# Kernel optimization log

Measured on AMD Instinct MI355X. Metric: run time of the kernel, lower is better.

## Reference

```python
import jax, jax.numpy as jnp
import numpy as np

SEQ_LEN, BATCH = 512, 64
VOCAB, EMB, HID = 10000, 512, 512


def _lstm_layer(x, Wih, Whh, bih, bhh):
    # x: [T, B, in_dim]; PyTorch gate order: i, f, g, o
    T, B, _ = x.shape
    H = Whh.shape[1]
    b = bih + bhh
    # precompute input projections for all timesteps: [T, B, 4H]
    xW = jnp.einsum('tbe,ge->tbg', x, Wih) + b

    def step(carry, xt):
        h, c = carry
        gates = xt + h @ Whh.T  # [B, 4H]
        i, f, g, o = jnp.split(gates, 4, axis=-1)
        i = jax.nn.sigmoid(i)
        f = jax.nn.sigmoid(f)
        g = jnp.tanh(g)
        o = jax.nn.sigmoid(o)
        c = f * c + i * g
        h = o * jnp.tanh(c)
        return (h, c), h

    init = (jnp.zeros((B, H), x.dtype), jnp.zeros((B, H), x.dtype))
    _, ys = jax.lax.scan(step, init, xW)
    return ys  # [T, B, H]


def setup_inputs() -> dict:
    key = jax.random.key(0)
    ks = jax.random.split(key, 12)
    src = jax.random.randint(ks[0], (SEQ_LEN, BATCH), 0, VOCAB)
    sen_len = jax.random.randint(ks[1], (BATCH,), 1, SEQ_LEN + 1)
    s_e = 1.0 / np.sqrt(EMB)
    s_h = 1.0 / np.sqrt(HID)
    emb_table = jax.random.normal(ks[2], (VOCAB, EMB), jnp.float32) * s_e
    Wih0 = jax.random.uniform(ks[3], (4 * HID, EMB), jnp.float32, -s_h, s_h)
    Whh0 = jax.random.uniform(ks[4], (4 * HID, HID), jnp.float32, -s_h, s_h)
    bih0 = jax.random.uniform(ks[5], (4 * HID,), jnp.float32, -s_h, s_h)
    bhh0 = jax.random.uniform(ks[6], (4 * HID,), jnp.float32, -s_h, s_h)
    Wih1 = jax.random.uniform(ks[7], (4 * HID, HID), jnp.float32, -s_h, s_h)
    Whh1 = jax.random.uniform(ks[8], (4 * HID, HID), jnp.float32, -s_h, s_h)
    bih1 = jax.random.uniform(ks[9], (4 * HID,), jnp.float32, -s_h, s_h)
    bhh1 = jax.random.uniform(ks[10], (4 * HID,), jnp.float32, -s_h, s_h)
    return {"src": src, "sen_len": sen_len, "emb_table": emb_table,
            "Wih0": Wih0, "Whh0": Whh0, "bih0": bih0, "bhh0": bhh0,
            "Wih1": Wih1, "Whh1": Whh1, "bih1": bih1, "bhh1": bhh1}


def reference(src, sen_len, emb_table, Wih0, Whh0, bih0, bhh0, Wih1, Whh1, bih1, bhh1):
    # Vectorized embedding gather: [T, B, EMB]
    embedded = emb_table[src]
    # Two-layer LSTM (eval mode; inter-layer dropout inactive)
    h1 = _lstm_layer(embedded, Wih0, Whh0, bih0, bhh0)
    outputs = _lstm_layer(h1, Wih1, Whh1, bih1, bhh1)  # [T, B, HID]
    # Per-sequence last valid hidden state, concatenated into flat vector [B*HID]
    B = src.shape[1]
    ot = outputs[sen_len - 1, jnp.arange(B), :]  # [B, HID]
    return ot.reshape(-1)
```

## Files before the change

### kernel.cpp

```cpp
#include <hip/hip_runtime.h>

#define T_LEN 512
#define BATCH 64
#define HID   512
#define EMB   512
#define NWG   256
#define TPB   512
#define RING_SLOT (HID * BATCH)

struct GBar {
  int leaf[16 * 32];
  int root; int pad1[31];
  int epoch; int pad2[31];
  int gep[16 * 32];
};

__global__ void init_ws_kernel(int* ws, int n) {
  int stride = gridDim.x * blockDim.x;
  for (int i = blockIdx.x * blockDim.x + threadIdx.x; i < n; i += stride) ws[i] = 0;
}

__device__ __forceinline__ float sigm(float x)      { return 1.f / (1.f + __expf(-x)); }
__device__ __forceinline__ float tanh_fast(float x) { return 1.f - 2.f / (__expf(2.f * x) + 1.f); }

__device__ __forceinline__ void cstore(float* p, float v) {
  __hip_atomic_store(p, v, __ATOMIC_RELAXED, __HIP_MEMORY_SCOPE_AGENT);
}

template <int I, int N>
struct Issue16 {
  static __device__ __forceinline__ void go(float4* dst, const float* p) {
    asm volatile("global_load_dwordx4 %0, %1, off offset:%2 sc0 sc1"
                 : "=v"(dst[I]) : "v"(p), "i"(I * 256));
    Issue16<I + 1, N>::go(dst, p);
  }
};
template <int N>
struct Issue16<N, N> {
  static __device__ __forceinline__ void go(float4*, const float*) {}
};

#define WAIT_VM(n) do {                                     \
    __builtin_amdgcn_sched_barrier(0);                      \
    asm volatile("s_waitcnt vmcnt(" #n ")" ::: "memory");   \
    __builtin_amdgcn_sched_barrier(0);                      \
  } while (0)

#define DOT_ACC(a, xv, wv) \
  a = fmaf((xv).w, (wv).w, fmaf((xv).z, (wv).z, fmaf((xv).y, (wv).y, fmaf((xv).x, (wv).x, (a)))))
#define AXPY4(acc, s, v) do { \
  (acc).x = fmaf((s), (v).x, (acc).x); \
  (acc).y = fmaf((s), (v).y, (acc).y); \
  (acc).z = fmaf((s), (v).z, (acc).z); \
  (acc).w = fmaf((s), (v).w, (acc).w); } while (0)

__global__ __launch_bounds__(TPB, 2) void lstm_pipe(
    const int* __restrict__ src, const int* __restrict__ sen_len,
    const float* __restrict__ emb,
    const float* __restrict__ Wih0, const float* __restrict__ Whh0,
    const float* __restrict__ bih0, const float* __restrict__ bhh0,
    const float* __restrict__ Wih1, const float* __restrict__ Whh1,
    const float* __restrict__ bih1, const float* __restrict__ bhh1,
    float* __restrict__ out,
    int* __restrict__ barp, float* __restrict__ h0ring, float* __restrict__ h1ring)
{
  extern __shared__ char smem_raw[];
  float4* WlV  = (float4*)smem_raw;
  float*  part = (float*)(smem_raw + 65536);
  GBar* bar = (GBar*)barp;

  const int wg    = blockIdx.x;
  const int layer = wg >> 7;
  const int w     = wg & 127;
  const int tid   = threadIdx.x;
  const int kh    = tid >> 6;
  const int lane  = tid & 63;
  const int bg    = lane >> 2;
  const int rg    = lane & 3;
  const int b0    = bg << 2;
  const int k0    = kh << 7;

  const float* Wih = layer ? Wih1 : Wih0;
  const float* Whh = layer ? Whh1 : Whh0;

  for (int idx = tid; idx < 4096; idx += TPB) {
    int rowl = idx & 15;
    int kc   = idx >> 4;
    int q = rowl >> 2, rjj = rowl & 3;
    int grow = q * HID + (w << 2) + rjj;
    int k4 = kc << 2;
    float4 v;
    if (k4 < EMB) v = *(const float4*)(Wih + (size_t)grow * EMB + k4);
    else          v = *(const float4*)(Whh + (size_t)grow * HID + (k4 - EMB));
    WlV[kc * 16 + rowl] = v;
  }

  const int p_b  = tid & 63;
  const int p_jj = (tid >> 6) & 3;
  const int p_jg = (w << 2) + p_jj;
  float bias4[4] = {0.f, 0.f, 0.f, 0.f};
  float c = 0.f;
  int   slen = -2;
  if (tid < 256) {
#pragma unroll
    for (int q = 0; q < 4; ++q) {
      int r = q * HID + p_jg;
      bias4[q] = layer ? (bih1[r] + bhh1[r]) : (bih0[r] + bhh0[r]);
    }
    slen = sen_len[p_b];
  }
  __syncthreads();

  for (int s = 0; s <= T_LEN; ++s) {
    const bool active = (layer == 0) ? (s < T_LEN) : (s >= 1);
    if (active) {
      const int t = (layer == 0) ? s : (s - 1);
      float4 acc[4];
#pragma unroll
      for (int q = 0; q < 4; ++q) acc[q] = make_float4(0.f, 0.f, 0.f, 0.f);

      if (layer == 0 && kh < 4) {
        const int* st = src + t * BATCH + b0;
        const float* e0 = emb + (size_t)st[0] * EMB;
        const float* e1 = emb + (size_t)st[1] * EMB;
        const float* e2 = emb + (size_t)st[2] * EMB;
        const float* e3 = emb + (size_t)st[3] * EMB;
#pragma unroll 4
        for (int kk = 0; kk < 128; kk += 4) {
          const int k  = k0 + kk;
          const int kc = k >> 2;
          float4 x0 = *(const float4*)(e0 + k);
          float4 x1 = *(const float4*)(e1 + k);
          float4 x2 = *(const float4*)(e2 + k);
          float4 x3 = *(const float4*)(e3 + k);
#pragma unroll
          for (int q = 0; q < 4; ++q) {
            float4 wq = WlV[kc * 16 + (q << 2) + rg];
            DOT_ACC(acc[q].x, x0, wq);
            DOT_ACC(acc[q].y, x1, wq);
            DOT_ACC(acc[q].z, x2, wq);
            DOT_ACC(acc[q].w, x3, wq);
          }
        }
      } else {
        const float* xT;
        if (layer == 0) {
          xT = h0ring + ((s + 1) & 1) * RING_SLOT + (k0 - EMB) * BATCH;
        } else if (kh < 4) {
          xT = h0ring + ((s - 1) & 1) * RING_SLOT + k0 * BATCH;
        } else {
          xT = h1ring + ((s - 1) & 1) * RING_SLOT + (k0 - EMB) * BATCH;
        }
        const float* p = xT + b0;

        float4 xa[16], xb[16];
        Issue16<0, 16>::go(xa, p);
#pragma unroll
        for (int g = 0; g < 8; ++g) {
          float4* cur = (g & 1) ? xb : xa;
          float4* nxt = (g & 1) ? xa : xb;
          if (g < 7) {
            Issue16<0, 16>::go(nxt, p + (g + 1) * 16 * BATCH);
            WAIT_VM(16);
          } else {
            WAIT_VM(0);
          }
#pragma unroll
          for (int ib = 0; ib < 4; ++ib) {
            const int kc = (k0 + (g << 4) + (ib << 2)) >> 2;
#pragma unroll
            for (int q = 0; q < 4; ++q) {
              float4 wq = WlV[kc * 16 + (q << 2) + rg];
              AXPY4(acc[q], wq.x, cur[(ib << 2) + 0]);
              AXPY4(acc[q], wq.y, cur[(ib << 2) + 1]);
              AXPY4(acc[q], wq.z, cur[(ib << 2) + 2]);
              AXPY4(acc[q], wq.w, cur[(ib << 2) + 3]);
            }
          }
        }
      }
#pragma unroll
      for (int q = 0; q < 4; ++q)
        *(float4*)(part + (kh << 10) + (((q << 2) + rg) << 6) + b0) = acc[q];
    }

    __syncthreads();

    if (active && tid < 256) {
      float g4[4];
#pragma unroll
      for (int q = 0; q < 4; ++q) {
        float a = bias4[q];
        const int base = (((q << 2) + p_jj) << 6) + p_b;
#pragma unroll
        for (int kk = 0; kk < 8; ++kk) a += part[(kk << 10) + base];
        g4[q] = a;
      }
      float ig = sigm(g4[0]), fg = sigm(g4[1]), gg = tanh_fast(g4[2]), og = sigm(g4[3]);
      c = fmaf(fg, c, ig * gg);
      float h = og * tanh_fast(c);
      float* ring = (layer == 0 ? h0ring : h1ring) + (s & 1) * RING_SLOT;
      cstore(ring + p_jg * BATCH + p_b, h);
      if (layer == 1) {
        const int t = s - 1;
        if (t == slen - 1) out[p_b * HID + p_jg] = h;
      }
    }

    __syncthreads();
    if (tid == 0) {
      const int target = s + 1;
      int* leafp = &bar->leaf[(wg >> 4) * 32];
      int* gepp  = &bar->gep[(wg >> 4) * 32];
      int prev = __hip_atomic_fetch_add(leafp, 1, __ATOMIC_RELAXED, __HIP_MEMORY_SCOPE_AGENT);
      if ((prev & 15) == 15) {
        int r = __hip_atomic_fetch_add(&bar->root, 1, __ATOMIC_RELAXED, __HIP_MEMORY_SCOPE_AGENT);
        if ((r & 15) == 15) {
          __hip_atomic_store(&bar->epoch, target, __ATOMIC_RELAXED, __HIP_MEMORY_SCOPE_AGENT);
        } else {
          while (__hip_atomic_load(&bar->epoch, __ATOMIC_RELAXED, __HIP_MEMORY_SCOPE_AGENT) < target)
            __builtin_amdgcn_s_sleep(1);
        }
        __hip_atomic_store(gepp, target, __ATOMIC_RELAXED, __HIP_MEMORY_SCOPE_AGENT);
      } else {
        while (__hip_atomic_load(gepp, __ATOMIC_RELAXED, __HIP_MEMORY_SCOPE_AGENT) < target)
          __builtin_amdgcn_s_sleep(1);
      }
    }
    __syncthreads();
  }
}

extern "C" void kernel_launch(void* const* d_in, const int* in_sizes, int n_in,
                              void* d_out, int out_size, void* d_ws, size_t ws_size,
                              hipStream_t stream) {
  const int*   src  = (const int*)d_in[0];
  const int*   slen = (const int*)d_in[1];
  const float* emb  = (const float*)d_in[2];
  const float* Wih0 = (const float*)d_in[3];
  const float* Whh0 = (const float*)d_in[4];
  const float* bih0 = (const float*)d_in[5];
  const float* bhh0 = (const float*)d_in[6];
  const float* Wih1 = (const float*)d_in[7];
  const float* Whh1 = (const float*)d_in[8];
  const float* bih1 = (const float*)d_in[9];
  const float* bhh1 = (const float*)d_in[10];
  float* out = (float*)d_out;

  int*   bar    = (int*)d_ws;
  float* h0ring = (float*)((char*)d_ws + 8192);
  float* h1ring = h0ring + 2 * RING_SLOT;

  int zero_ints = (8192 + 4 * RING_SLOT * 4) / 4;
  hipLaunchKernelGGL(init_ws_kernel, dim3(64), dim3(256), 0, stream, (int*)d_ws, zero_ints);

  (void)hipFuncSetAttribute((const void*)lstm_pipe,
                            hipFuncAttributeMaxDynamicSharedMemorySize, 98304);

  hipLaunchKernelGGL(lstm_pipe, dim3(NWG), dim3(TPB), 98304, stream,
                     src, slen, emb, Wih0, Whh0, bih0, bhh0, Wih1, Whh1, bih1, bhh1,
                     out, bar, h0ring, h1ring);
}
```

Before: 5.829 ms.

## Swizzle LDS weights, split K across lanes with DPP reduction, flatten barrier wait

Weights in LDS are stored with an XOR-like rotation so that lanes in a row group read different banks. In the recurrent ring path, each of the 4 lanes of a row group now covers a quarter of K across all 16 rows instead of 4 rows over full K. The partial sums are combined with DPP quad reductions, and only lane 0 of each group writes the result. The grid barrier drops the per-group epoch broadcast, so every workgroup polls the single global epoch directly, which removes one hop of latency but puts more pollers on one address. The change also raises register pressure with 16 float4 accumulators.

```diff
diff --git a/kernel.cpp b/kernel.cpp
--- a/kernel.cpp
+++ b/kernel.cpp
@@ -27,16 +27,24 @@
   __hip_atomic_store(p, v, __ATOMIC_RELAXED, __HIP_MEMORY_SCOPE_AGENT);
 }
 
+__device__ __forceinline__ float qsum(float v) {
+  int t = __builtin_amdgcn_update_dpp(0, __float_as_int(v), 0xB1, 0xF, 0xF, false);
+  v += __int_as_float(t);
+  t = __builtin_amdgcn_update_dpp(0, __float_as_int(v), 0x4E, 0xF, 0xF, false);
+  v += __int_as_float(t);
+  return v;
+}
+
 template <int I, int N>
-struct Issue16 {
+struct IssueQ {
   static __device__ __forceinline__ void go(float4* dst, const float* p) {
     asm volatile("global_load_dwordx4 %0, %1, off offset:%2 sc0 sc1"
                  : "=v"(dst[I]) : "v"(p), "i"(I * 256));
-    Issue16<I + 1, N>::go(dst, p);
+    IssueQ<I + 1, N>::go(dst, p);
   }
 };
 template <int N>
-struct Issue16<N, N> {
+struct IssueQ<N, N> {
   static __device__ __forceinline__ void go(float4*, const float*) {}
 };
 
@@ -92,8 +100,19 @@
     float4 v;
     if (k4 < EMB) v = *(const float4*)(Wih + (size_t)grow * EMB + k4);
     else          v = *(const float4*)(Whh + (size_t)grow * HID + (k4 - EMB));
-    WlV[kc * 16 + rowl] = v;
-  }
+    int slot = (rowl + 2 * ((kc >> 3) & 3)) & 15;
+    WlV[kc * 16 + slot] = v;
+  }
+
+  const bool embmode = (layer == 0) && (kh < 4);
+  int toff[16];
+  {
+    const int add = embmode ? rg : (rg << 1);
+#pragma unroll
+    for (int i = 0; i < 16; ++i) toff[i] = ((i + add) & 15) << 4;
+  }
+  const char* wb_ring = (const char*)smem_raw + (size_t)((kh << 5) + (rg << 3)) * 256;
+  const char* wb_emb  = (const char*)smem_raw + (size_t)(kh << 13);
 
   const int p_b  = tid & 63;
   const int p_jj = (tid >> 6) & 3;
@@ -115,33 +134,36 @@
     const bool active = (layer == 0) ? (s < T_LEN) : (s >= 1);
     if (active) {
       const int t = (layer == 0) ? s : (s - 1);
-      float4 acc[4];
-#pragma unroll
-      for (int q = 0; q < 4; ++q) acc[q] = make_float4(0.f, 0.f, 0.f, 0.f);
-
-      if (layer == 0 && kh < 4) {
+
+      if (embmode) {
+        float4 acc[4];
+#pragma unroll
+        for (int q = 0; q < 4; ++q) acc[q] = make_float4(0.f, 0.f, 0.f, 0.f);
         const int* st = src + t * BATCH + b0;
         const float* e0 = emb + (size_t)st[0] * EMB;
         const float* e1 = emb + (size_t)st[1] * EMB;
         const float* e2 = emb + (size_t)st[2] * EMB;
         const float* e3 = emb + (size_t)st[3] * EMB;
-#pragma unroll 4
+#pragma unroll
         for (int kk = 0; kk < 128; kk += 4) {
+          const int sw = (kk >> 5) & 3;
           const int k  = k0 + kk;
-          const int kc = k >> 2;
           float4 x0 = *(const float4*)(e0 + k);
           float4 x1 = *(const float4*)(e1 + k);
           float4 x2 = *(const float4*)(e2 + k);
           float4 x3 = *(const float4*)(e3 + k);
 #pragma unroll
           for (int q = 0; q < 4; ++q) {
-            float4 wq = WlV[kc * 16 + (q << 2) + rg];
+            float4 wq = *(const float4*)(wb_emb + kk * 64 + toff[((q << 2) + 2 * sw) & 15]);
             DOT_ACC(acc[q].x, x0, wq);
             DOT_ACC(acc[q].y, x1, wq);
             DOT_ACC(acc[q].z, x2, wq);
             DOT_ACC(acc[q].w, x3, wq);
           }
         }
+#pragma unroll
+        for (int q = 0; q < 4; ++q)
+          *(float4*)(part + (kh << 10) + (((q << 2) + rg) << 6) + b0) = acc[q];
       } else {
         const float* xT;
         if (layer == 0) {
@@ -151,37 +173,51 @@
         } else {
           xT = h1ring + ((s - 1) & 1) * RING_SLOT + (k0 - EMB) * BATCH;
         }
-        const float* p = xT + b0;
-
-        float4 xa[16], xb[16];
-        Issue16<0, 16>::go(xa, p);
-#pragma unroll
-        for (int g = 0; g < 8; ++g) {
-          float4* cur = (g & 1) ? xb : xa;
-          float4* nxt = (g & 1) ? xa : xb;
-          if (g < 7) {
-            Issue16<0, 16>::go(nxt, p + (g + 1) * 16 * BATCH);
-            WAIT_VM(16);
-          } else {
-            WAIT_VM(0);
-          }
-#pragma unroll
-          for (int ib = 0; ib < 4; ++ib) {
-            const int kc = (k0 + (g << 4) + (ib << 2)) >> 2;
-#pragma unroll
-            for (int q = 0; q < 4; ++q) {
-              float4 wq = WlV[kc * 16 + (q << 2) + rg];
-              AXPY4(acc[q], wq.x, cur[(ib << 2) + 0]);
-              AXPY4(acc[q], wq.y, cur[(ib << 2) + 1]);
-              AXPY4(acc[q], wq.z, cur[(ib << 2) + 2]);
-              AXPY4(acc[q], wq.w, cur[(ib << 2) + 3]);
-            }
-          }
-        }
-      }
-#pragma unroll
-      for (int q = 0; q < 4; ++q)
-        *(float4*)(part + (kh << 10) + (((q << 2) + rg) << 6) + b0) = acc[q];
+        const float* p = xT + (rg << 5) * BATCH + b0;
+
+        float4 acc[16];
+#pragma unroll
+        for (int m = 0; m < 16; ++m) acc[m] = make_float4(0.f, 0.f, 0.f, 0.f);
+
+        float4 xa[8], xb[8];
+        IssueQ<0, 8>::go(xa, p);
+
+#define RING_GRP(G, CUR, NXT, WN, DO_ISSUE)                                   \
+        do {                                                                  \
+          if (DO_ISSUE) IssueQ<0, 8>::go(NXT, p + ((G) + 1) * 8 * BATCH);     \
+          WAIT_VM(WN);                                                        \
+          _Pragma("unroll")                                                   \
+          for (int cc = 0; cc < 2; ++cc) {                                    \
+            _Pragma("unroll")                                                 \
+            for (int m = 0; m < 16; ++m) {                                    \
+              float4 wq = *(const float4*)(wb_ring + ((G) * 2 + cc) * 256 + toff[m]); \
+              AXPY4(acc[m], wq.x, (CUR)[cc * 4 + 0]);                         \
+              AXPY4(acc[m], wq.y, (CUR)[cc * 4 + 1]);                         \
+              AXPY4(acc[m], wq.z, (CUR)[cc * 4 + 2]);                         \
+              AXPY4(acc[m], wq.w, (CUR)[cc * 4 + 3]);                         \
+            }                                                                 \
+          }                                                                   \
+        } while (0)
+
+        RING_GRP(0, xa, xb, 8, true);
+        RING_GRP(1, xb, xa, 8, true);
+        RING_GRP(2, xa, xb, 8, true);
+        RING_GRP(3, xb, xa, 0, false);
+#undef RING_GRP
+
+#pragma unroll
+        for (int m = 0; m < 16; ++m) {
+          acc[m].x = qsum(acc[m].x);
+          acc[m].y = qsum(acc[m].y);
+          acc[m].z = qsum(acc[m].z);
+          acc[m].w = qsum(acc[m].w);
+        }
+        if (rg == 0) {
+#pragma unroll
+          for (int m = 0; m < 16; ++m)
+            *(float4*)(part + (kh << 10) + (m << 6) + b0) = acc[m];
+        }
+      }
     }
 
     __syncthreads();
@@ -211,19 +247,17 @@
     if (tid == 0) {
       const int target = s + 1;
       int* leafp = &bar->leaf[(wg >> 4) * 32];
-      int* gepp  = &bar->gep[(wg >> 4) * 32];
       int prev = __hip_atomic_fetch_add(leafp, 1, __ATOMIC_RELAXED, __HIP_MEMORY_SCOPE_AGENT);
+      bool winner = false;
       if ((prev & 15) == 15) {
         int r = __hip_atomic_fetch_add(&bar->root, 1, __ATOMIC_RELAXED, __HIP_MEMORY_SCOPE_AGENT);
         if ((r & 15) == 15) {
           __hip_atomic_store(&bar->epoch, target, __ATOMIC_RELAXED, __HIP_MEMORY_SCOPE_AGENT);
-        } else {
-          while (__hip_atomic_load(&bar->epoch, __ATOMIC_RELAXED, __HIP_MEMORY_SCOPE_AGENT) < target)
-            __builtin_amdgcn_s_sleep(1);
-        }
-        __hip_atomic_store(gepp, target, __ATOMIC_RELAXED, __HIP_MEMORY_SCOPE_AGENT);
-      } else {
-        while (__hip_atomic_load(gepp, __ATOMIC_RELAXED, __HIP_MEMORY_SCOPE_AGENT) < target)
+          winner = true;
+        }
+      }
+      if (!winner) {
+        while (__hip_atomic_load(&bar->epoch, __ATOMIC_RELAXED, __HIP_MEMORY_SCOPE_AGENT) < target)
           __builtin_amdgcn_s_sleep(1);
       }
     }
```

Result: slower. 15.50 ms (+165.9%).
